# Optimization experiments

Measured on AMD Instinct MI355X. Metric: run time of the kernel, lower is better.

The kernel has to match this reference:

```python
import jax, jax.numpy as jnp
import numpy as np

N_BLOCKS, N_LAYERS = 3, 10
RW, SW = 256, 128          # residual_width, skip_width
COND_DIM = 16
OUT_CH = 256
K = 3                      # kernel_size (odd)
B, L = 1, 4096             # L divisible by max dilation 512
NL = N_BLOCKS * N_LAYERS
DILATIONS = [2 ** l for _ in range(N_BLOCKS) for l in range(N_LAYERS)] + [1]


def dilate(x, new, old):
    # WaveNet dilate trick: (n, c, l) -> (n*new/old, c, l*old/new) by
    # permute->reshape->permute (matches torch permute(1,2,0).view(c,l2,n2).permute(2,0,1)).
    n, c, l = x.shape
    if new == old:
        return x
    n2 = n * new // old
    l2 = l * old // new
    return jnp.transpose(jnp.transpose(x, (1, 2, 0)).reshape(c, l2, n2), (2, 0, 1))


def conv1d(x, w, b=None, pad=0):
    y = jax.lax.conv_general_dilated(x, w, (1,), [(pad, pad)],
                                     dimension_numbers=('NCH', 'OIH', 'NCH'))
    if b is not None:
        y = y + b[None, :, None]
    return y


def setup_inputs() -> dict:
    key = jax.random.key(0)
    ks = jax.random.split(key, 14)
    s = 0.05
    return {
        'x': jax.random.normal(ks[0], (B, 1, L), jnp.float32),
        'conditionals': jax.random.normal(ks[1], (B, COND_DIM, L), jnp.float32),
        'init_w': jax.random.normal(ks[2], (RW, 1, K), jnp.float32) * s,
        'init_b': jnp.zeros((RW,), jnp.float32),
        'init_skip_w': jax.random.normal(ks[3], (SW, RW, 1), jnp.float32) * s,
        'init_skip_b': jnp.zeros((SW,), jnp.float32),
        'filter_w': jax.random.normal(ks[4], (NL, RW, RW, K), jnp.float32) * s,
        'gate_w': jax.random.normal(ks[5], (NL, RW, RW, K), jnp.float32) * s,
        'skip_w': jax.random.normal(ks[6], (NL, SW, RW, 1), jnp.float32) * s,
        'feat_w': jax.random.normal(ks[7], (NL, RW, RW, 1), jnp.float32) * s,
        'fcond_w': jax.random.normal(ks[8], (NL, RW, COND_DIM, 1), jnp.float32) * s,
        'gcond_w': jax.random.normal(ks[9], (NL, RW, COND_DIM, 1), jnp.float32) * s,
        'final_skip_w': jax.random.normal(ks[10], (SW, SW, 1), jnp.float32) * s,
        'final_skip_b': jnp.zeros((SW,), jnp.float32),
        'final_w': jax.random.normal(ks[11], (OUT_CH, SW, 1), jnp.float32) * s,
        'final_b': jnp.zeros((OUT_CH,), jnp.float32),
    }


def reference(x, conditionals, init_w, init_b, init_skip_w, init_skip_b,
              filter_w, gate_w, skip_w, feat_w, fcond_w, gcond_w,
              final_skip_w, final_skip_b, final_w, final_b):
    pad = (K - 1) // 2
    feat = conv1d(x, init_w, init_b, pad=pad)          # (B, RW, L)
    skip = conv1d(feat, init_skip_w, init_skip_b)       # (B, SW, L)
    for i in range(NL):
        d = DILATIONS[i]
        dilated = dilate(feat, d, DILATIONS[i - 1])     # (B*d, RW, L/d)
        f = conv1d(dilated, filter_w[i], pad=pad)
        g = conv1d(dilated, gate_w[i], pad=pad)
        # 1x1 conditioning convs (no bias) on (B, COND_DIM, L), then dilate to match
        cf = jnp.einsum('oi,bil->bol', fcond_w[i, :, :, 0], conditionals)
        cg = jnp.einsum('oi,bil->bol', gcond_w[i, :, :, 0], conditionals)
        f = f + dilate(cf, d, 1)
        g = g + dilate(cg, d, 1)
        residual = jax.nn.sigmoid(f) * jnp.tanh(g)
        feat = dilated + conv1d(residual, feat_w[i])    # residual connection
        skip = skip + dilate(conv1d(residual, skip_w[i]), 1, d)  # undilate skip
    skip = conv1d(jax.nn.relu(skip), final_skip_w, final_skip_b)
    out = conv1d(jax.nn.relu(skip), final_w, final_b)   # (B, OUT_CH, L)
    return out
```

## Files before the change

### kernel.cpp

```cpp
#include <hip/hip_runtime.h>
#include <cstddef>
#include <cstdint>

#define L_LEN 4096
#define RWID 256
#define SWID 128
#define NLAY 30

typedef __attribute__((ext_vector_type(8))) short bf16x8;
typedef __attribute__((ext_vector_type(4))) float f32x4;

__device__ __forceinline__ ushort f2bf(float x) {
  union { float f; uint32_t u; } v; v.f = x;
  uint32_t r = v.u + 0x7fffu + ((v.u >> 16) & 1u);
  return (ushort)(r >> 16);
}

__device__ __forceinline__ void gload16(const void* g, void* l) {
  __builtin_amdgcn_global_load_lds(
      (const __attribute__((address_space(1))) void*)g,
      (__attribute__((address_space(3))) void*)l, 16, 0, 0);
}

__device__ __forceinline__ f32x4 mfma16(bf16x8 a, bf16x8 b, f32x4 c) {
  return __builtin_amdgcn_mfma_f32_16x16x32_bf16(a, b, c, 0, 0, 0);
}

__global__ __launch_bounds__(256) void prep_wres(
    const float* __restrict__ filter_w, const float* __restrict__ gate_w,
    const float* __restrict__ fcond_w, const float* __restrict__ gcond_w,
    ushort* __restrict__ wres)
{
  const int idx = blockIdx.x * 256 + threadIdx.x;
  const int k = idx % 800;
  int rest = idx / 800;
  const int co = rest & 255; rest >>= 8;
  const int fg = rest & 1;
  const int i = rest >> 1;
  float v;
  if (k < 768) {
    const int tap = k >> 8, cin = k & 255;
    const float* s = fg ? gate_w : filter_w;
    v = s[(((size_t)i * 256 + co) * 256 + cin) * 3 + tap];
  } else if (k < 784) {
    const float* s = fg ? gcond_w : fcond_w;
    v = s[((size_t)i * 256 + co) * 16 + (k - 768)];
  } else v = 0.f;
  wres[idx] = f2bf(v);
}

__global__ __launch_bounds__(256) void prep_wu(
    const float* __restrict__ feat_w, const float* __restrict__ skip_w,
    ushort* __restrict__ wu)
{
  const int idx = blockIdx.x * 256 + threadIdx.x;
  const int rc = idx & 255;
  const int rest = idx >> 8;
  const int m = rest % 384;
  const int i = rest / 384;
  float v = (m < 256) ? feat_w[((size_t)i * 256 + m) * 256 + rc]
                      : skip_w[((size_t)i * 128 + (m - 256)) * 256 + rc];
  wu[idx] = f2bf(v);
}

__global__ __launch_bounds__(256) void prep_misc(
    const float* __restrict__ cond, const float* __restrict__ isw,
    const float* __restrict__ fsw, const float* __restrict__ fw,
    ushort* __restrict__ condT, ushort* __restrict__ wisk,
    ushort* __restrict__ wfsk, ushort* __restrict__ wfin,
    ushort* __restrict__ zerobuf)
{
  const int idx = blockIdx.x * 256 + threadIdx.x;
  if (idx < 131072) {
    const int t = idx >> 5, cd = idx & 31;
    condT[idx] = (cd < 16) ? f2bf(cond[(size_t)cd * L_LEN + t]) : (ushort)0;
  } else if (idx < 131072 + 32768) {
    const int j = idx - 131072; wisk[j] = f2bf(isw[j]);
  } else if (idx < 131072 + 32768 + 16384) {
    const int j = idx - (131072 + 32768); wfsk[j] = f2bf(fsw[j]);
  } else if (idx < 131072 + 32768 + 16384 + 32768) {
    const int j = idx - (131072 + 32768 + 16384); wfin[j] = f2bf(fw[j]);
  } else if (idx < 131072 + 32768 + 16384 + 32768 + 512) {
    zerobuf[idx - (131072 + 32768 + 16384 + 32768)] = 0;
  }
}

__global__ __launch_bounds__(256) void init_feat(
    const float* __restrict__ x, const float* __restrict__ w,
    const float* __restrict__ b, float* __restrict__ featT_f32,
    ushort* __restrict__ featT_bf16)
{
  const int t = blockIdx.x, c = threadIdx.x;
  const float xm = (t > 0) ? x[t - 1] : 0.f;
  const float x0 = x[t];
  const float xp = (t < L_LEN - 1) ? x[t + 1] : 0.f;
  const float v = b[c] + w[c * 3] * xm + w[c * 3 + 1] * x0 + w[c * 3 + 2] * xp;
  featT_f32[(size_t)t * 256 + c] = v;
  featT_bf16[(size_t)t * 256 + c] = f2bf(v);
}

__global__ __launch_bounds__(256) void residual_mfma(
    const ushort* __restrict__ featT,
    const ushort* __restrict__ condT,
    const ushort* __restrict__ wres,
    const ushort* __restrict__ zerobuf,
    ushort* __restrict__ resT,
    int d)
{
  __shared__ ushort lds[2][4096];
  const int t0  = blockIdx.x * 64;
  const int co0 = blockIdx.y * 32;
  const int tid = threadIdx.x;
  const int lane = tid & 63;
  const int w    = tid >> 6;

  const int srow = lane >> 2;
  const int soct = (lane & 3) ^ ((srow >> 1) & 3);

  const int fgA  = w >> 1;
  const int arow = ((w & 1) << 4) + srow;
  const ushort* asrc0 = wres + ((size_t)fgA * 256 + (co0 + arow)) * 800 + soct * 8;
  const int aLds = fgA * 1024 + (w & 1) * 512;
  const int bLds = 2048 + w * 512;

  const int rl   = lane & 15;
  const int octr = (lane >> 4) ^ ((rl >> 1) & 3);
  const int aoff = rl * 32 + octr * 8;
  const int boff = 2048 + (w * 16 + rl) * 32 + octr * 8;

  f32x4 accf[2] = {}; f32x4 accg[2] = {};

  auto stage = [&](int kc, int buf) {
    const int k0 = kc * 32;
    gload16(asrc0 + k0, &lds[buf][aLds]);
    const int rB = w * 16 + srow;
    const ushort* bsrc;
    if (kc < 24) {
      const int tap = kc >> 3, cin0 = (kc & 7) * 32;
      const int tt = t0 + rB + (tap - 1) * d;
      bsrc = (tt >= 0 && tt < L_LEN)
               ? featT + (size_t)tt * 256 + cin0 + soct * 8
               : zerobuf;
    } else {
      bsrc = condT + (size_t)(t0 + rB) * 32 + soct * 8;
    }
    gload16(bsrc, &lds[buf][bLds]);
  };

  stage(0, 0);
  __syncthreads();
  for (int kc = 0; kc < 25; ++kc) {
    const int cur = kc & 1;
    if (kc + 1 < 25) stage(kc + 1, cur ^ 1);
    const ushort* base = lds[cur];
    bf16x8 af0 = *(const bf16x8*)(base + aoff);
    bf16x8 af1 = *(const bf16x8*)(base + aoff + 512);
    bf16x8 ag0 = *(const bf16x8*)(base + aoff + 1024);
    bf16x8 ag1 = *(const bf16x8*)(base + aoff + 1536);
    bf16x8 b0  = *(const bf16x8*)(base + boff);
    accf[0] = mfma16(af0, b0, accf[0]);
    accf[1] = mfma16(af1, b0, accf[1]);
    accg[0] = mfma16(ag0, b0, accg[0]);
    accg[1] = mfma16(ag1, b0, accg[1]);
    __syncthreads();
  }

  const int cobase = co0 + (lane >> 4) * 4;
  const int t = t0 + w * 16 + rl;
#pragma unroll
  for (int m = 0; m < 2; ++m) {
    const f32x4 f = accf[m], g = accg[m];
    ushort4 ov;
    float o[4];
#pragma unroll
    for (int r = 0; r < 4; ++r) {
      const float ff = f[r], gg = g[r];
      const float sig = 1.f / (1.f + __expf(-ff));
      const float ag2 = fabsf(gg);
      float th = 1.f - 2.f / (__expf(2.f * ag2) + 1.f);
      th = (gg < 0.f) ? -th : th;
      o[r] = sig * th;
    }
    ov.x = f2bf(o[0]); ov.y = f2bf(o[1]); ov.z = f2bf(o[2]); ov.w = f2bf(o[3]);
    *(ushort4*)&resT[(size_t)t * 256 + cobase + m * 16] = ov;
  }
}

__global__ __launch_bounds__(256) void update_mfma(
    const ushort* __restrict__ resT,
    const ushort* __restrict__ wu,
    float* __restrict__ featT_f32, ushort* __restrict__ featT_bf16,
    float* __restrict__ skipT_f32)
{
  __shared__ ushort lds[2][3072];
  const int t0 = blockIdx.x * 64;
  const int m0 = blockIdx.y * 32;
  const int tid = threadIdx.x;
  const int lane = tid & 63;
  const int w    = tid >> 6;

  const int srow = lane >> 2;
  const int soct = (lane & 3) ^ ((srow >> 1) & 3);

  const ushort* asrc0 = wu + (size_t)(m0 + (w & 1) * 16 + srow) * 256 + soct * 8;
  const int aLds = (w & 1) * 512;
  const int bLds = 1024 + w * 512;

  const int rl   = lane & 15;
  const int octr = (lane >> 4) ^ ((rl >> 1) & 3);
  const int aoff = rl * 32 + octr * 8;
  const int boff = 1024 + (w * 16 + rl) * 32 + octr * 8;

  f32x4 acc[2] = {};

  auto stage = [&](int kc, int buf) {
    const int k0 = kc * 32;
    if (w < 2) gload16(asrc0 + k0, &lds[buf][aLds]);
    const int rB = w * 16 + srow;
    gload16(resT + (size_t)(t0 + rB) * 256 + k0 + soct * 8, &lds[buf][bLds]);
  };

  stage(0, 0);
  __syncthreads();
  for (int kc = 0; kc < 8; ++kc) {
    const int cur = kc & 1;
    if (kc + 1 < 8) stage(kc + 1, cur ^ 1);
    const ushort* base = lds[cur];
    bf16x8 a0 = *(const bf16x8*)(base + aoff);
    bf16x8 a1 = *(const bf16x8*)(base + aoff + 512);
    bf16x8 b0 = *(const bf16x8*)(base + boff);
    acc[0] = mfma16(a0, b0, acc[0]);
    acc[1] = mfma16(a1, b0, acc[1]);
    __syncthreads();
  }

  const int mbase = m0 + (lane >> 4) * 4;
  const int t = t0 + w * 16 + rl;
#pragma unroll
  for (int m = 0; m < 2; ++m) {
    const int mm = mbase + m * 16;
    const f32x4 a = acc[m];
    if (m0 < 256) {
      float4* p = (float4*)&featT_f32[(size_t)t * 256 + mm];
      float4 v = *p;
      v.x += a[0]; v.y += a[1]; v.z += a[2]; v.w += a[3];
      *p = v;
      ushort4 ov; ov.x = f2bf(v.x); ov.y = f2bf(v.y); ov.z = f2bf(v.z); ov.w = f2bf(v.w);
      *(ushort4*)&featT_bf16[(size_t)t * 256 + mm] = ov;
    } else {
      float4* p = (float4*)&skipT_f32[(size_t)t * 128 + (mm - 256)];
      float4 v = *p;
      v.x += a[0]; v.y += a[1]; v.z += a[2]; v.w += a[3];
      *p = v;
    }
  }
}

template<int MODE, int KLEN>
__global__ __launch_bounds__(256) void gemm_mfma(
    const ushort* __restrict__ A,
    const ushort* __restrict__ B,
    const float* __restrict__ bias,
    void* __restrict__ outp)
{
  __shared__ ushort lds[2][3072];
  const int t0 = blockIdx.x * 64;
  const int m0 = blockIdx.y * 32;
  const int tid = threadIdx.x;
  const int lane = tid & 63;
  const int w    = tid >> 6;

  const int srow = lane >> 2;
  const int soct = (lane & 3) ^ ((srow >> 1) & 3);

  const ushort* asrc0 = A + (size_t)(m0 + (w & 1) * 16 + srow) * KLEN + soct * 8;
  const int aLds = (w & 1) * 512;
  const int bLds = 1024 + w * 512;

  const int rl   = lane & 15;
  const int octr = (lane >> 4) ^ ((rl >> 1) & 3);
  const int aoff = rl * 32 + octr * 8;
  const int boff = 1024 + (w * 16 + rl) * 32 + octr * 8;

  f32x4 acc[2] = {};
  constexpr int KSTEPS = KLEN / 32;

  auto stage = [&](int kc, int buf) {
    const int k0 = kc * 32;
    if (w < 2) gload16(asrc0 + k0, &lds[buf][aLds]);
    const int rB = w * 16 + srow;
    gload16(B + (size_t)(t0 + rB) * KLEN + k0 + soct * 8, &lds[buf][bLds]);
  };

  stage(0, 0);
  __syncthreads();
  for (int kc = 0; kc < KSTEPS; ++kc) {
    const int cur = kc & 1;
    if (kc + 1 < KSTEPS) stage(kc + 1, cur ^ 1);
    const ushort* base = lds[cur];
    bf16x8 a0 = *(const bf16x8*)(base + aoff);
    bf16x8 a1 = *(const bf16x8*)(base + aoff + 512);
    bf16x8 b0 = *(const bf16x8*)(base + boff);
    acc[0] = mfma16(a0, b0, acc[0]);
    acc[1] = mfma16(a1, b0, acc[1]);
    __syncthreads();
  }

  const int mbase = m0 + (lane >> 4) * 4;
  const int t = t0 + w * 16 + rl;
#pragma unroll
  for (int m = 0; m < 2; ++m) {
    const int mm = mbase + m * 16;
    const float4 bb = *(const float4*)&bias[mm];
    const f32x4 a = acc[m];
    float o[4] = {a[0] + bb.x, a[1] + bb.y, a[2] + bb.z, a[3] + bb.w};
    if (MODE == 0) {
      *(float4*)&((float*)outp)[(size_t)t * 128 + mm] = make_float4(o[0], o[1], o[2], o[3]);
    } else if (MODE == 1) {
      ushort4 ov;
      ov.x = f2bf(fmaxf(o[0], 0.f)); ov.y = f2bf(fmaxf(o[1], 0.f));
      ov.z = f2bf(fmaxf(o[2], 0.f)); ov.w = f2bf(fmaxf(o[3], 0.f));
      *(ushort4*)&((ushort*)outp)[(size_t)t * 128 + mm] = ov;
    } else {
      float* op = (float*)outp;
#pragma unroll
      for (int r = 0; r < 4; ++r) op[(size_t)(mm + r) * L_LEN + t] = o[r];
    }
  }
}

__global__ __launch_bounds__(256) void relu_cvt(
    const float* __restrict__ in, ushort* __restrict__ outv, int n4)
{
  const int i = blockIdx.x * 256 + threadIdx.x;
  if (i >= n4) return;
  const float4 v = ((const float4*)in)[i];
  ushort4 o;
  o.x = f2bf(fmaxf(v.x, 0.f)); o.y = f2bf(fmaxf(v.y, 0.f));
  o.z = f2bf(fmaxf(v.z, 0.f)); o.w = f2bf(fmaxf(v.w, 0.f));
  ((ushort4*)outv)[i] = o;
}

extern "C" void kernel_launch(void* const* d_in, const int* in_sizes, int n_in,
                              void* d_out, int out_size, void* d_ws, size_t ws_size,
                              hipStream_t stream) {
  const float* x            = (const float*)d_in[0];
  const float* cond         = (const float*)d_in[1];
  const float* init_w       = (const float*)d_in[2];
  const float* init_b       = (const float*)d_in[3];
  const float* init_skip_w  = (const float*)d_in[4];
  const float* init_skip_b  = (const float*)d_in[5];
  const float* filter_w     = (const float*)d_in[6];
  const float* gate_w       = (const float*)d_in[7];
  const float* skip_w       = (const float*)d_in[8];
  const float* feat_w       = (const float*)d_in[9];
  const float* fcond_w      = (const float*)d_in[10];
  const float* gcond_w      = (const float*)d_in[11];
  const float* final_skip_w = (const float*)d_in[12];
  const float* final_skip_b = (const float*)d_in[13];
  const float* final_w      = (const float*)d_in[14];
  const float* final_b      = (const float*)d_in[15];
  float* out = (float*)d_out;
  (void)in_sizes; (void)n_in; (void)out_size; (void)ws_size;

  char* ws = (char*)d_ws;
  size_t off = 0;
  auto alloc = [&](size_t bytes) { void* p = ws + off; off = (off + bytes + 255) & ~(size_t)255; return p; };
  float*  featT_f32  = (float*) alloc((size_t)L_LEN * 256 * 4);
  ushort* featT_bf16 = (ushort*)alloc((size_t)L_LEN * 256 * 2);
  ushort* resT       = (ushort*)alloc((size_t)L_LEN * 256 * 2);
  float*  skipT_f32  = (float*) alloc((size_t)L_LEN * 128 * 4);
  ushort* skipR      = (ushort*)alloc((size_t)L_LEN * 128 * 2);
  ushort* skip2R     = (ushort*)alloc((size_t)L_LEN * 128 * 2);
  ushort* condT      = (ushort*)alloc((size_t)L_LEN * 32 * 2);
  ushort* wres       = (ushort*)alloc((size_t)NLAY * 2 * 256 * 800 * 2);
  ushort* wu         = (ushort*)alloc((size_t)NLAY * 384 * 256 * 2);
  ushort* wisk       = (ushort*)alloc((size_t)128 * 256 * 2);
  ushort* wfsk       = (ushort*)alloc((size_t)128 * 128 * 2);
  ushort* wfin       = (ushort*)alloc((size_t)256 * 128 * 2);
  ushort* zerobuf    = (ushort*)alloc(1024);

  const dim3 B256(256);
  prep_wres<<<48000, B256, 0, stream>>>(filter_w, gate_w, fcond_w, gcond_w, wres);
  prep_wu<<<11520, B256, 0, stream>>>(feat_w, skip_w, wu);
  prep_misc<<<833, B256, 0, stream>>>(cond, init_skip_w, final_skip_w, final_w,
                                      condT, wisk, wfsk, wfin, zerobuf);
  init_feat<<<L_LEN, B256, 0, stream>>>(x, init_w, init_b, featT_f32, featT_bf16);
  gemm_mfma<0, 256><<<dim3(64, 4), B256, 0, stream>>>(wisk, featT_bf16, init_skip_b, skipT_f32);

  for (int i = 0; i < NLAY; ++i) {
    const int d = 1 << (i % 10);
    residual_mfma<<<dim3(64, 8), B256, 0, stream>>>(
        featT_bf16, condT, wres + (size_t)i * 2 * 256 * 800, zerobuf, resT, d);
    update_mfma<<<dim3(64, 12), B256, 0, stream>>>(
        resT, wu + (size_t)i * 384 * 256, featT_f32, featT_bf16, skipT_f32);
  }

  relu_cvt<<<512, B256, 0, stream>>>(skipT_f32, skipR, (L_LEN * 128) / 4);
  gemm_mfma<1, 128><<<dim3(64, 4), B256, 0, stream>>>(wfsk, skipR, final_skip_b, skip2R);
  gemm_mfma<2, 128><<<dim3(64, 8), B256, 0, stream>>>(wfin, skip2R, final_b, out);
}
```

Baseline: 722.8 us.

## Triple-buffer LDS staging with explicit vmcnt waits in MFMA kernels

Moves the residual, update and generic GEMM kernels from double-buffered to triple-buffered LDS staging, prefetching two k-chunks ahead. The __syncthreads calls are replaced by partial s_waitcnt vmcnt waits plus raw s_barrier, so later global-to-LDS loads can stay in flight across iterations. The aim is to hide global load latency behind the MFMA work. In exchange it uses more LDS per block and relies on hand-counted vmcnt values, which break if the per-wave load counts in stage() change.

Result: faster. 635.0 us (-12.1%).

```diff
diff --git a/kernel.cpp b/kernel.cpp
--- a/kernel.cpp
+++ b/kernel.cpp
@@ -24,6 +24,15 @@
 
 __device__ __forceinline__ f32x4 mfma16(bf16x8 a, bf16x8 b, f32x4 c) {
   return __builtin_amdgcn_mfma_f32_16x16x32_bf16(a, b, c, 0, 0, 0);
+}
+
+template<int N> __device__ __forceinline__ void waitvm() {
+  asm volatile("s_waitcnt vmcnt(%0)" :: "i"(N) : "memory");
+}
+__device__ __forceinline__ void blockbar() {
+  __builtin_amdgcn_sched_barrier(0);
+  asm volatile("s_barrier" ::: "memory");
+  __builtin_amdgcn_sched_barrier(0);
 }
 
 __global__ __launch_bounds__(256) void prep_wres(
@@ -107,7 +116,7 @@
     ushort* __restrict__ resT,
     int d)
 {
-  __shared__ ushort lds[2][4096];
+  __shared__ ushort lds[3][4096];
   const int t0  = blockIdx.x * 64;
   const int co0 = blockIdx.y * 32;
   const int tid = threadIdx.x;
@@ -148,11 +157,13 @@
   };
 
   stage(0, 0);
-  __syncthreads();
+  stage(1, 1);
   for (int kc = 0; kc < 25; ++kc) {
-    const int cur = kc & 1;
-    if (kc + 1 < 25) stage(kc + 1, cur ^ 1);
-    const ushort* base = lds[cur];
+    if (kc + 2 < 25) { stage(kc + 2, (kc + 2) % 3); waitvm<4>(); }
+    else if (kc + 1 < 25) waitvm<2>();
+    else waitvm<0>();
+    blockbar();
+    const ushort* base = lds[kc % 3];
     bf16x8 af0 = *(const bf16x8*)(base + aoff);
     bf16x8 af1 = *(const bf16x8*)(base + aoff + 512);
     bf16x8 ag0 = *(const bf16x8*)(base + aoff + 1024);
@@ -162,7 +173,7 @@
     accf[1] = mfma16(af1, b0, accf[1]);
     accg[0] = mfma16(ag0, b0, accg[0]);
     accg[1] = mfma16(ag1, b0, accg[1]);
-    __syncthreads();
+    blockbar();
   }
 
   const int cobase = co0 + (lane >> 4) * 4;
@@ -192,7 +203,7 @@
     float* __restrict__ featT_f32, ushort* __restrict__ featT_bf16,
     float* __restrict__ skipT_f32)
 {
-  __shared__ ushort lds[2][3072];
+  __shared__ ushort lds[3][3072];
   const int t0 = blockIdx.x * 64;
   const int m0 = blockIdx.y * 32;
   const int tid = threadIdx.x;
@@ -212,6 +223,7 @@
   const int boff = 1024 + (w * 16 + rl) * 32 + octr * 8;
 
   f32x4 acc[2] = {};
+  const bool twoLoads = (w < 2);
 
   auto stage = [&](int kc, int buf) {
     const int k0 = kc * 32;
@@ -221,17 +233,22 @@
   };
 
   stage(0, 0);
-  __syncthreads();
+  stage(1, 1);
   for (int kc = 0; kc < 8; ++kc) {
-    const int cur = kc & 1;
-    if (kc + 1 < 8) stage(kc + 1, cur ^ 1);
-    const ushort* base = lds[cur];
+    if (kc + 2 < 8) {
+      stage(kc + 2, (kc + 2) % 3);
+      if (twoLoads) waitvm<4>(); else waitvm<2>();
+    } else if (kc + 1 < 8) {
+      if (twoLoads) waitvm<2>(); else waitvm<1>();
+    } else waitvm<0>();
+    blockbar();
+    const ushort* base = lds[kc % 3];
     bf16x8 a0 = *(const bf16x8*)(base + aoff);
     bf16x8 a1 = *(const bf16x8*)(base + aoff + 512);
     bf16x8 b0 = *(const bf16x8*)(base + boff);
     acc[0] = mfma16(a0, b0, acc[0]);
     acc[1] = mfma16(a1, b0, acc[1]);
-    __syncthreads();
+    blockbar();
   }
 
   const int mbase = m0 + (lane >> 4) * 4;
@@ -263,7 +280,7 @@
     const float* __restrict__ bias,
     void* __restrict__ outp)
 {
-  __shared__ ushort lds[2][3072];
+  __shared__ ushort lds[3][3072];
   const int t0 = blockIdx.x * 64;
   const int m0 = blockIdx.y * 32;
   const int tid = threadIdx.x;
@@ -283,7 +300,8 @@
   const int boff = 1024 + (w * 16 + rl) * 32 + octr * 8;
 
   f32x4 acc[2] = {};
-  constexpr int KSTEPS = KLEN / 32;
+  constexpr int NC = KLEN / 32;
+  const bool twoLoads = (w < 2);
 
   auto stage = [&](int kc, int buf) {
     const int k0 = kc * 32;
@@ -293,17 +311,22 @@
   };
 
   stage(0, 0);
-  __syncthreads();
-  for (int kc = 0; kc < KSTEPS; ++kc) {
-    const int cur = kc & 1;
-    if (kc + 1 < KSTEPS) stage(kc + 1, cur ^ 1);
-    const ushort* base = lds[cur];
+  stage(1, 1);
+  for (int kc = 0; kc < NC; ++kc) {
+    if (kc + 2 < NC) {
+      stage(kc + 2, (kc + 2) % 3);
+      if (twoLoads) waitvm<4>(); else waitvm<2>();
+    } else if (kc + 1 < NC) {
+      if (twoLoads) waitvm<2>(); else waitvm<1>();
+    } else waitvm<0>();
+    blockbar();
+    const ushort* base = lds[kc % 3];
     bf16x8 a0 = *(const bf16x8*)(base + aoff);
     bf16x8 a1 = *(const bf16x8*)(base + aoff + 512);
     bf16x8 b0 = *(const bf16x8*)(base + boff);
     acc[0] = mfma16(a0, b0, acc[0]);
     acc[1] = mfma16(a1, b0, acc[1]);
-    __syncthreads();
+    blockbar();
   }
 
   const int mbase = m0 + (lane >> 4) * 4;
```
